# Kernel optimization log

Hardware: AMD Instinct MI355X
Metric: run time of the kernel (lower is better)

Reference implementation:

```python
import jax, jax.numpy as jnp
import numpy as np

NSIDE = 128
NLAT = 4 * NSIDE - 1          # 511 iso-latitude rings
NLON = 4 * NSIDE              # max pixels per ring (equatorial belt)
LMAX = NLAT                   # 511
MMAX = NLON // 2 + 1          # 257
NPIX = 12 * NSIDE * NSIDE     # 196608 HEALPix pixels (RING ordering)


def _healpix_geometry(nside, mmax):
    """Precompute per-ring synthesis tables for the irregular HEALPix iFFT.

    For ring k with nphi_k pixels and phase offset o_k, pixel longitudes are
    phi_{k,j} = 2*pi*(j + o_k)/nphi_k.  Real synthesis from one-sided spectrum:
        f_{k,j} = sum_m w_m * (Re(c_{k,m}) cos(m phi) - Im(c_{k,m}) sin(m phi)),
    w_0 = 1, w_m = 2 for m > 0 (irfft, norm='forward' convention as in
    torch-harmonics style SHT synthesis).  Returns dense [nlat, nlon, mmax]
    cos/sin tables masked to each ring's true length, plus the flat gather
    index mapping RING-ordered pixels into the padded [nlat, nlon] grid.
    """
    N = nside
    nlat, nlon = 4 * N - 1, 4 * N
    k = np.arange(nlat)
    # ring sizes: polar caps 4*i pixels, equatorial belt 4*N pixels
    nphi = np.where(k < N - 1, 4 * (k + 1),
                    np.where(k > 3 * N - 1, 4 * (4 * N - 1 - k), 4 * N))
    # phase offsets: caps shifted by half a pixel; belt alternates 1/2, 0
    off = np.where((k < N - 1) | (k > 3 * N - 1), 0.5,
                   np.where(((k - (N - 1)) % 2) == 0, 0.5, 0.0))
    j = np.arange(nlon)
    mask = (j[None, :] < nphi[:, None]).astype(np.float32)          # [nlat, nlon]
    phi = (2.0 * np.pi) * (j[None, :] + off[:, None]) / nphi[:, None]
    m = np.arange(mmax)
    w = np.where(m == 0, 1.0, 2.0).astype(np.float32)               # one-sided weights
    ang = (phi[:, :, None] * m[None, None, :]).astype(np.float32)   # [nlat, nlon, mmax]
    A = (w * np.cos(ang)) * mask[:, :, None]
    B = (-w * np.sin(ang)) * mask[:, :, None]
    # RING-ordered flat pixel -> (ring, j) -> padded-grid flat index
    starts = np.concatenate([[0], np.cumsum(nphi)[:-1]])
    ring = np.repeat(np.arange(nlat), nphi)
    jj = np.arange(int(nphi.sum())) - starts[ring]
    fidx = (ring * nlon + jj).astype(np.int32)
    return A.astype(np.float32), B.astype(np.float32), fidx


def setup_inputs() -> dict:
    key = jax.random.key(0)
    kx, kp = jax.random.split(key)
    # spectral coefficients, real view of complex [..., lmax, mmax]
    x = jax.random.normal(kx, (4, 16, LMAX, MMAX, 2), dtype=jnp.float32)
    # associated Legendre table buffer pct[m, l, k_ring] (random stand-in;
    # the real module precomputes normalized Legendre polynomials here)
    pct = jax.random.normal(kp, (MMAX, LMAX, NLAT), dtype=jnp.float32) * 0.05
    A, B, fidx = _healpix_geometry(NSIDE, MMAX)
    return {
        "x": x,
        "pct": pct,
        "A": jnp.asarray(A),
        "B": jnp.asarray(B),
        "fidx": jnp.asarray(fidx),
    }


def reference(x, pct, A, B, fidx):
    xr, xi = x[..., 0], x[..., 1]                       # [..., lmax, mmax]
    # Legendre contraction: '...lmn,mlk->...kmn' on the real view is simply
    # the same real contraction applied to Re and Im independently.
    Xr = jnp.einsum('...lm,mlk->...km', xr, pct)        # [..., nlat, mmax]
    Xi = jnp.einsum('...lm,mlk->...km', xi, pct)
    # irregular per-ring real iFFT synthesis on padded [nlat, nlon] grid
    grid = jnp.einsum('kjm,...km->...kj', A, Xr) + jnp.einsum('kjm,...km->...kj', B, Xi)
    flat = grid.reshape(grid.shape[:-2] + (NLAT * NLON,))
    return flat[..., fidx]                              # [..., npix] RING order
```

## Files before the change

### kernel.cpp

```cpp
#include <hip/hip_runtime.h>
#include <cstddef>

#define NSIDE_ 128
#define NLAT_  511
#define NLON_  512
#define LMAX_  511
#define MMAX_  257
#define NPIX_  196608
#define NB_    64
#define TWO_PI_ 6.28318530717958647692f

#define XELEMS_   16809856u
#define X2TELEMS_ 16842752u

typedef __attribute__((ext_vector_type(8))) short bf16x8;
typedef __attribute__((ext_vector_type(4))) float f32x4;

static __device__ __forceinline__ unsigned short f2bf(float f) {
    union { float f; unsigned int u; } v; v.f = f;
    unsigned int r = v.u + 0x7FFFu + ((v.u >> 16) & 1u);
    return (unsigned short)(r >> 16);
}

static __device__ __forceinline__ unsigned int cvtpk(float lo, float hi) {
    unsigned int d;
    asm("v_cvt_pk_bf16_f32 %0, %1, %2" : "=v"(d) : "v"(lo), "v"(hi));
    return d;
}

union U4V { uint4 u; bf16x8 v; };

static __device__ __forceinline__ bf16x8 ld_b64x2(const unsigned int* p) {
    union { struct { uint2 a, b; } s; bf16x8 v; } t;
    t.s.a = *(const uint2*)p;
    t.s.b = *(const uint2*)(p + 2);
    return t.v;
}

__global__ __launch_bounds__(256) void pack_x_k(
    const float* __restrict__ x, unsigned short* __restrict__ x2T)
{
    __shared__ unsigned short lds[32][520];
    int b   = blockIdx.x;
    int l0  = blockIdx.y * 32;
    int tid = threadIdx.x;

    const float* src = x + ((size_t)b * LMAX_ + l0) * (2 * MMAX_);
    for (int li = 0; li < 32; ++li) {
        bool valid = (l0 + li) < LMAX_;
        for (int m2 = tid; m2 < 2 * MMAX_; m2 += 256) {
            float f = valid ? src[(size_t)li * (2 * MMAX_) + m2] : 0.f;
            lds[li][m2] = f2bf(f);
        }
    }
    __syncthreads();

    for (int m2 = tid; m2 < 2 * MMAX_; m2 += 256) {
        int m  = m2 >> 1;
        int rb = (m2 & 1) * 64 + b;
        unsigned short* dst = x2T + ((size_t)m * 128 + rb) * 512 + l0;
#pragma unroll
        for (int g = 0; g < 4; ++g) {
            unsigned int w0 = (unsigned int)lds[g*8+0][m2] | ((unsigned int)lds[g*8+1][m2] << 16);
            unsigned int w1 = (unsigned int)lds[g*8+2][m2] | ((unsigned int)lds[g*8+3][m2] << 16);
            unsigned int w2 = (unsigned int)lds[g*8+4][m2] | ((unsigned int)lds[g*8+5][m2] << 16);
            unsigned int w3 = (unsigned int)lds[g*8+6][m2] | ((unsigned int)lds[g*8+7][m2] << 16);
            *(uint4*)(dst + g * 8) = make_uint4(w0, w1, w2, w3);
        }
    }
}

__global__ __launch_bounds__(256, 3) void legendre4_k(
    const unsigned short* __restrict__ x2T,
    const float* __restrict__ pct,
    float* __restrict__ X)
{
    int kt = blockIdx.x, m = blockIdx.y;
    int k0 = kt * 128;
    int lane = threadIdx.x & 63, w = threadIdx.x >> 6;
    int wk = (w >> 1) * 64, wrb = (w & 1) * 64;
    int r = lane & 15, g = lane >> 4;

    const float* pctm = pct + (size_t)m * (LMAX_ * NLAT_);
    const unsigned short* x2m = x2T + (size_t)m * (128 * 512);

    f32x4 acc[4][4];
#pragma unroll
    for (int a = 0; a < 4; ++a)
#pragma unroll
        for (int c = 0; c < 4; ++c) acc[a][c] = (f32x4){0.f, 0.f, 0.f, 0.f};

    int krow[4];
#pragma unroll
    for (int ks = 0; ks < 4; ++ks) {
        int k = k0 + wk + ks * 16 + r;
        krow[ks] = (k < NLAT_) ? k : (NLAT_ - 1);
    }

#pragma unroll 1
    for (int ls = 0; ls < 16; ++ls) {
        int lbase = ls * 32 + g * 8;

        bf16x8 Bf[4];
#pragma unroll
        for (int rs = 0; rs < 4; ++rs)
            Bf[rs] = *(const bf16x8*)(x2m + ((size_t)(wrb + rs * 16 + r) * 512 + lbase));

        bf16x8 Af[4];
#pragma unroll
        for (int ks = 0; ks < 4; ++ks) {
            float t[8];
#pragma unroll
            for (int i = 0; i < 8; ++i) {
                int l = lbase + i;
                if (l > LMAX_ - 1) l = LMAX_ - 1;
                t[i] = pctm[(size_t)l * NLAT_ + krow[ks]];
            }
            U4V uv;
            uv.u.x = cvtpk(t[0], t[1]);
            uv.u.y = cvtpk(t[2], t[3]);
            uv.u.z = cvtpk(t[4], t[5]);
            uv.u.w = cvtpk(t[6], t[7]);
            Af[ks] = uv.v;
        }

#pragma unroll
        for (int ks = 0; ks < 4; ++ks)
#pragma unroll
            for (int rs = 0; rs < 4; ++rs)
                acc[ks][rs] = __builtin_amdgcn_mfma_f32_16x16x32_bf16(
                    Af[ks], Bf[rs], acc[ks][rs], 0, 0, 0);
    }

    float wgt = (m == 0) ? 1.f : 2.f;
#pragma unroll
    for (int ks = 0; ks < 4; ++ks) {
#pragma unroll
        for (int rs = 0; rs < 4; ++rs) {
            int rb = wrb + rs * 16 + r;
#pragma unroll
            for (int i = 0; i < 4; ++i) {
                int k = k0 + wk + ks * 16 + g * 4 + i;
                if (k < NLAT_)
                    X[((size_t)k * MMAX_ + m) * 128 + rb] = acc[ks][rs][i] * wgt;
            }
        }
    }
}

__global__ __launch_bounds__(256, 3) void synth4_k(
    const float* __restrict__ X,
    float* __restrict__ out)
{
    __shared__ __align__(16) unsigned int Adw[256 * 18];
    __shared__ __align__(16) unsigned int Bdw[64 * 18];

    int k  = blockIdx.x;
    int jh = blockIdx.y;

    int nphi, start; float off;
    if (k < NSIDE_ - 1) {
        nphi  = 4 * (k + 1);
        start = 2 * k * (k + 1);
        off   = 0.5f;
    } else if (k <= 3 * NSIDE_ - 1) {
        nphi  = 4 * NSIDE_;
        start = 2 * (NSIDE_ - 1) * NSIDE_ + (k - (NSIDE_ - 1)) * 4 * NSIDE_;
        off   = (((k - (NSIDE_ - 1)) & 1) == 0) ? 0.5f : 0.f;
    } else {
        int t = NLAT_ - k;
        nphi  = 4 * t;
        start = NPIX_ - 2 * t * (t + 1);
        off   = 0.5f;
    }
    int jblk = jh * 256;
    if (jblk >= nphi) return;

    int tid  = threadIdx.x;
    int lane = tid & 63, w = tid >> 6;
    int r = lane & 15, g = lane >> 4;

    float theta = TWO_PI_ * ((float)(jblk + tid) + off) / (float)nphi;
    float dc, ds;
    sincosf(theta, &ds, &dc);
    float cs = 1.f, sn = 0.f;

    int bb = tid & 63, kq = tid >> 6;
    const float* Xk = X + (size_t)k * (MMAX_ * 128) + bb;
    float bv[8];
#pragma unroll
    for (int i = 0; i < 8; ++i) {
        int kap = kq * 8 + i;
        bv[i] = Xk[(size_t)(kap >> 1) * 128 + (kap & 1) * 64];
    }

    bool wact = (jblk + w * 64) < nphi;

    f32x4 acc[4][4];
#pragma unroll
    for (int a = 0; a < 4; ++a)
#pragma unroll
        for (int c = 0; c < 4; ++c) acc[a][c] = (f32x4){0.f, 0.f, 0.f, 0.f};

#pragma unroll 1
    for (int s = 0; s < 17; ++s) {
        unsigned int adw[16];
#pragma unroll
        for (int mi = 0; mi < 16; ++mi) {
            adw[mi] = cvtpk(cs, -sn);
            float cn = fmaf(cs, dc, -(sn * ds));
            float s2 = fmaf(sn, dc,  cs * ds);
            cs = cn; sn = s2;
        }
        unsigned int bdw[4];
#pragma unroll
        for (int q = 0; q < 4; ++q) bdw[q] = cvtpk(bv[2 * q], bv[2 * q + 1]);

        __syncthreads();
        {
            unsigned int* ap = Adw + tid * 18;
#pragma unroll
            for (int q = 0; q < 8; ++q)
                *(uint2*)(ap + 2 * q) = make_uint2(adw[2 * q], adw[2 * q + 1]);
            unsigned int* bp = Bdw + bb * 18 + kq * 4;
            *(uint2*)bp       = make_uint2(bdw[0], bdw[1]);
            *(uint2*)(bp + 2) = make_uint2(bdw[2], bdw[3]);
        }
        if (s + 1 < 17) {
            int kap0 = (s + 1) * 32 + kq * 8;
#pragma unroll
            for (int i = 0; i < 8; ++i) {
                int kap = kap0 + i;
                int mm  = kap >> 1;
                bv[i] = (mm < MMAX_) ? Xk[(size_t)mm * 128 + (kap & 1) * 64] : 0.f;
            }
        }
        __syncthreads();

        if (wact) {
            bf16x8 Af[4], Bf[4];
#pragma unroll
            for (int ks = 0; ks < 4; ++ks)
                Af[ks] = ld_b64x2(Adw + (w * 64 + ks * 16 + r) * 18 + g * 4);
#pragma unroll
            for (int bs = 0; bs < 4; ++bs)
                Bf[bs] = ld_b64x2(Bdw + (bs * 16 + r) * 18 + g * 4);
#pragma unroll
            for (int ks = 0; ks < 4; ++ks)
#pragma unroll
                for (int bs = 0; bs < 4; ++bs)
                    acc[ks][bs] = __builtin_amdgcn_mfma_f32_16x16x32_bf16(
                        Af[ks], Bf[bs], acc[ks][bs], 0, 0, 0);
        }
    }

    if (wact) {
#pragma unroll
        for (int ks = 0; ks < 4; ++ks)
#pragma unroll
            for (int bs = 0; bs < 4; ++bs) {
                int b = bs * 16 + r;
#pragma unroll
                for (int i = 0; i < 4; ++i) {
                    int j = jblk + w * 64 + ks * 16 + g * 4 + i;
                    if (j < nphi)
                        out[(size_t)b * NPIX_ + start + j] = acc[ks][bs][i];
                }
            }
    }
}

__global__ __launch_bounds__(256) void legendre_k(
    const float* __restrict__ x,
    const float* __restrict__ pct,
    float* __restrict__ X)
{
    int k  = blockIdx.x * 256 + threadIdx.x;
    int m  = blockIdx.y;
    int bh = blockIdx.z;
    bool active = (k < NLAT_);
    if (!active) k = NLAT_ - 1;

    float accR[32], accI[32];
#pragma unroll
    for (int i = 0; i < 32; ++i) { accR[i] = 0.f; accI[i] = 0.f; }

    const float* pcol  = pct + (size_t)m * LMAX_ * NLAT_ + k;
    const float* xbase = x + (size_t)(bh * 32) * LMAX_ * MMAX_ * 2 + (size_t)m * 2;
    const size_t bstride = (size_t)LMAX_ * MMAX_ * 2;

    for (int l = 0; l < LMAX_; ++l) {
        float p = pcol[(size_t)l * NLAT_];
        const float* xl = xbase + (size_t)l * MMAX_ * 2;
#pragma unroll
        for (int bb = 0; bb < 32; ++bb) {
            accR[bb] = fmaf(xl[(size_t)bb * bstride],     p, accR[bb]);
            accI[bb] = fmaf(xl[(size_t)bb * bstride + 1], p, accI[bb]);
        }
    }
    if (active) {
        float wv = (m == 0) ? 1.f : 2.f;
        size_t base = ((size_t)k * MMAX_ + m) * 128 + bh * 32;
#pragma unroll
        for (int bb = 0; bb < 32; ++bb) {
            X[base + bb]      = accR[bb] * wv;
            X[base + 64 + bb] = accI[bb] * wv;
        }
    }
}

__global__ __launch_bounds__(256) void synth2_k(
    const float* __restrict__ X,
    float* __restrict__ out)
{
    int k  = blockIdx.x;
    int j  = blockIdx.y * 256 + threadIdx.x;
    int bh = blockIdx.z;

    int nphi, start; float off;
    if (k < NSIDE_ - 1) {
        nphi  = 4 * (k + 1);
        start = 2 * k * (k + 1);
        off   = 0.5f;
    } else if (k <= 3 * NSIDE_ - 1) {
        nphi  = 4 * NSIDE_;
        start = 2 * (NSIDE_ - 1) * NSIDE_ + (k - (NSIDE_ - 1)) * 4 * NSIDE_;
        off   = (((k - (NSIDE_ - 1)) & 1) == 0) ? 0.5f : 0.f;
    } else {
        int t = NLAT_ - k;
        nphi  = 4 * t;
        start = NPIX_ - 2 * t * (t + 1);
        off   = 0.5f;
    }
    if (blockIdx.y == 1 && nphi <= 256) return;
    bool store_ok = (j < nphi);

    float ang = TWO_PI_ * ((float)j + off) / (float)nphi;
    float dsn, dcs;
    sincosf(ang, &dsn, &dcs);

    const float* Xk = X + (size_t)k * MMAX_ * 128 + bh * 32;

    float acc[32];
#pragma unroll
    for (int i = 0; i < 32; ++i) acc[i] = 0.f;

    float c = 1.f, s = 0.f;
    for (int m = 0; m < MMAX_; ++m) {
        const float* xm = Xk + (size_t)m * 128;
#pragma unroll
        for (int bb = 0; bb < 32; ++bb) {
            acc[bb] = fmaf(c, xm[bb], acc[bb]);
            acc[bb] = fmaf(-s, xm[64 + bb], acc[bb]);
        }
        float cn = fmaf(c, dcs, -(s * dsn));
        float s2 = fmaf(s, dcs,  (c * dsn));
        c = cn; s = s2;
    }

    if (store_ok) {
        float* op = out + (size_t)(bh * 32) * NPIX_ + start + j;
#pragma unroll
        for (int bb = 0; bb < 32; ++bb)
            op[(size_t)bb * NPIX_] = acc[bb];
    }
}

extern "C" void kernel_launch(void* const* d_in, const int* in_sizes, int n_in,
                              void* d_out, int out_size, void* d_ws, size_t ws_size,
                              hipStream_t stream)
{
    const float* x   = (const float*)d_in[0];
    const float* pct = (const float*)d_in[1];
    float* out = (float*)d_out;
    float* X   = (float*)d_ws;

    size_t need = (size_t)XELEMS_ * 4 + (size_t)X2TELEMS_ * 2;
    if (ws_size >= need) {
        unsigned short* x2T = (unsigned short*)(X + XELEMS_);
        pack_x_k<<<dim3(64, 16), dim3(256), 0, stream>>>(x, x2T);
        legendre4_k<<<dim3(4, MMAX_), dim3(256), 0, stream>>>(x2T, pct, X);
        synth4_k<<<dim3(NLAT_, 2), dim3(256), 0, stream>>>(X, out);
    } else {
        legendre_k<<<dim3(2, MMAX_, 2), dim3(256), 0, stream>>>(x, pct, X);
        synth2_k<<<dim3(NLAT_, 2, 2), dim3(256), 0, stream>>>(X, out);
    }
}
```

Before: 265.1 us.

## Stage Legendre table through swizzled LDS and double-buffer both GEMM kernels

The Legendre kernel now loads pct tiles with coalesced k-contiguous reads, packs them to bf16 in a double-buffered, XOR-swizzled LDS tile, and prefetches the next tile and x fragments while the MFMAs run. Blocks are remapped so consecutive m values spread across XCDs. The synthesis kernel double-buffers its A/B LDS tiles, drops one barrier per step, computes the next twiddle chunk while the current MFMAs run, and swizzles LDS columns to reduce bank conflicts. This removes strided uncoalesced pct gathers and barrier stalls, at the cost of more LDS and register pressure.

```diff
diff --git a/kernel.cpp b/kernel.cpp
--- a/kernel.cpp
+++ b/kernel.cpp
@@ -7,7 +7,6 @@
 #define LMAX_  511
 #define MMAX_  257
 #define NPIX_  196608
-#define NB_    64
 #define TWO_PI_ 6.28318530717958647692f
 
 #define XELEMS_   16809856u
@@ -28,9 +27,7 @@
     return d;
 }
 
-union U4V { uint4 u; bf16x8 v; };
-
-static __device__ __forceinline__ bf16x8 ld_b64x2(const unsigned int* p) {
+static __device__ __forceinline__ bf16x8 ld_pair(const unsigned int* p) {
     union { struct { uint2 a, b; } s; bf16x8 v; } t;
     t.s.a = *(const uint2*)p;
     t.s.b = *(const uint2*)(p + 2);
@@ -70,66 +67,97 @@
     }
 }
 
-__global__ __launch_bounds__(256, 3) void legendre4_k(
+__global__ __launch_bounds__(256, 3) void legendre5_k(
     const unsigned short* __restrict__ x2T,
     const float* __restrict__ pct,
     float* __restrict__ X)
 {
-    int kt = blockIdx.x, m = blockIdx.y;
-    int k0 = kt * 128;
-    int lane = threadIdx.x & 63, w = threadIdx.x >> 6;
+    __shared__ __align__(16) unsigned int Apk[2][128 * 18];
+
+    int bid = blockIdx.x;
+    int xcd = bid & 7, n = bid >> 3;
+    int kt = n & 3, mi = n >> 2;
+    int m = mi * 8 + xcd;
+    if (m >= MMAX_) return;
+
+    int k0  = kt * 128;
+    int tid = threadIdx.x;
+    int lane = tid & 63, w = tid >> 6;
     int wk = (w >> 1) * 64, wrb = (w & 1) * 64;
     int r = lane & 15, g = lane >> 4;
 
     const float* pctm = pct + (size_t)m * (LMAX_ * NLAT_);
     const unsigned short* x2m = x2T + (size_t)m * (128 * 512);
 
+    int kc = tid & 15;
+    int lp = tid >> 4;
+    int o7 = (k0 + kc + 112 <= NLAT_ - 1) ? 112 : (NLAT_ - 1 - (k0 + kc));
+
     f32x4 acc[4][4];
 #pragma unroll
     for (int a = 0; a < 4; ++a)
 #pragma unroll
         for (int c = 0; c < 4; ++c) acc[a][c] = (f32x4){0.f, 0.f, 0.f, 0.f};
 
-    int krow[4];
-#pragma unroll
-    for (int ks = 0; ks < 4; ++ks) {
-        int k = k0 + wk + ks * 16 + r;
-        krow[ks] = (k < NLAT_) ? k : (NLAT_ - 1);
-    }
-
-#pragma unroll 1
-    for (int ls = 0; ls < 16; ++ls) {
-        int lbase = ls * 32 + g * 8;
-
-        bf16x8 Bf[4];
+    float e0[8], e1[8];
+    bf16x8 Bfc[4], Bfn[4];
+
+    {
+        const float* pa = pctm + (size_t)(2 * lp)     * NLAT_ + k0 + kc;
+        const float* pb = pctm + (size_t)(2 * lp + 1) * NLAT_ + k0 + kc;
+#pragma unroll
+        for (int i = 0; i < 7; ++i) { e0[i] = pa[16 * i]; e1[i] = pb[16 * i]; }
+        e0[7] = pa[o7]; e1[7] = pb[o7];
 #pragma unroll
         for (int rs = 0; rs < 4; ++rs)
-            Bf[rs] = *(const bf16x8*)(x2m + ((size_t)(wrb + rs * 16 + r) * 512 + lbase));
-
+            Bfc[rs] = *(const bf16x8*)(x2m + (size_t)(wrb + rs * 16 + r) * 512 + g * 8);
+    }
+
+#pragma unroll 2
+    for (int s = 0; s < 16; ++s) {
+        const int bsel = s & 1;
+        unsigned int* wp = &Apk[bsel][0];
+#pragma unroll
+        for (int i = 0; i < 8; ++i) {
+            unsigned int dwv = cvtpk(e0[i], e1[i]);
+            int kk = kc + 16 * i;
+            wp[kk * 18 + (lp ^ ((i & 3) << 2))] = dwv;
+        }
+        __syncthreads();
+
+        if (s < 15) {
+            int l0n = (s + 1) * 32;
+            int la = l0n + 2 * lp, lb = la + 1;
+            if (lb > LMAX_ - 1) lb = LMAX_ - 1;
+            const float* pa = pctm + (size_t)la * NLAT_ + k0 + kc;
+            const float* pb = pctm + (size_t)lb * NLAT_ + k0 + kc;
+#pragma unroll
+            for (int i = 0; i < 7; ++i) { e0[i] = pa[16 * i]; e1[i] = pb[16 * i]; }
+            e0[7] = pa[o7]; e1[7] = pb[o7];
+            int lbase = l0n + g * 8;
+#pragma unroll
+            for (int rs = 0; rs < 4; ++rs)
+                Bfn[rs] = *(const bf16x8*)(x2m + (size_t)(wrb + rs * 16 + r) * 512 + lbase);
+        }
+
+        const unsigned int* rp = &Apk[bsel][0];
         bf16x8 Af[4];
 #pragma unroll
         for (int ks = 0; ks < 4; ++ks) {
-            float t[8];
-#pragma unroll
-            for (int i = 0; i < 8; ++i) {
-                int l = lbase + i;
-                if (l > LMAX_ - 1) l = LMAX_ - 1;
-                t[i] = pctm[(size_t)l * NLAT_ + krow[ks]];
-            }
-            U4V uv;
-            uv.u.x = cvtpk(t[0], t[1]);
-            uv.u.y = cvtpk(t[2], t[3]);
-            uv.u.z = cvtpk(t[4], t[5]);
-            uv.u.w = cvtpk(t[6], t[7]);
-            Af[ks] = uv.v;
-        }
-
+            int row = wk + ks * 16 + r;
+            Af[ks] = ld_pair(rp + row * 18 + ((g * 4) ^ ((ks & 3) << 2)));
+        }
 #pragma unroll
         for (int ks = 0; ks < 4; ++ks)
 #pragma unroll
             for (int rs = 0; rs < 4; ++rs)
                 acc[ks][rs] = __builtin_amdgcn_mfma_f32_16x16x32_bf16(
-                    Af[ks], Bf[rs], acc[ks][rs], 0, 0, 0);
+                    Af[ks], Bfc[rs], acc[ks][rs], 0, 0, 0);
+
+        if (s < 15) {
+#pragma unroll
+            for (int rs = 0; rs < 4; ++rs) Bfc[rs] = Bfn[rs];
+        }
     }
 
     float wgt = (m == 0) ? 1.f : 2.f;
@@ -148,12 +176,12 @@
     }
 }
 
-__global__ __launch_bounds__(256, 3) void synth4_k(
+__global__ __launch_bounds__(256, 3) void synth5_k(
     const float* __restrict__ X,
     float* __restrict__ out)
 {
-    __shared__ __align__(16) unsigned int Adw[256 * 18];
-    __shared__ __align__(16) unsigned int Bdw[64 * 18];
+    __shared__ __align__(16) unsigned int Adw[2][256 * 18];
+    __shared__ __align__(16) unsigned int Bdw[2][64 * 18];
 
     int k  = blockIdx.x;
     int jh = blockIdx.y;
@@ -187,12 +215,27 @@
 
     int bb = tid & 63, kq = tid >> 6;
     const float* Xk = X + (size_t)k * (MMAX_ * 128) + bb;
+
+    int swzA = ((tid >> 4) & 3) << 2;
+    int swzB = ((bb  >> 4) & 3) << 2;
+
     float bv[8];
 #pragma unroll
     for (int i = 0; i < 8; ++i) {
         int kap = kq * 8 + i;
         bv[i] = Xk[(size_t)(kap >> 1) * 128 + (kap & 1) * 64];
     }
+    unsigned int adw[16];
+#pragma unroll
+    for (int mi2 = 0; mi2 < 16; ++mi2) {
+        adw[mi2] = cvtpk(cs, -sn);
+        float cn = fmaf(cs, dc, -(sn * ds));
+        float s2 = fmaf(sn, dc,  cs * ds);
+        cs = cn; sn = s2;
+    }
+    unsigned int bdw[4];
+#pragma unroll
+    for (int q = 0; q < 4; ++q) bdw[q] = cvtpk(bv[2 * q], bv[2 * q + 1]);
 
     bool wact = (jblk + w * 64) < nphi;
 
@@ -202,31 +245,22 @@
 #pragma unroll
         for (int c = 0; c < 4; ++c) acc[a][c] = (f32x4){0.f, 0.f, 0.f, 0.f};
 
-#pragma unroll 1
+#pragma unroll 2
     for (int s = 0; s < 17; ++s) {
-        unsigned int adw[16];
-#pragma unroll
-        for (int mi = 0; mi < 16; ++mi) {
-            adw[mi] = cvtpk(cs, -sn);
-            float cn = fmaf(cs, dc, -(sn * ds));
-            float s2 = fmaf(sn, dc,  cs * ds);
-            cs = cn; sn = s2;
-        }
-        unsigned int bdw[4];
-#pragma unroll
-        for (int q = 0; q < 4; ++q) bdw[q] = cvtpk(bv[2 * q], bv[2 * q + 1]);
-
+        const int bsel = s & 1;
+        {
+            unsigned int* ap = &Adw[bsel][tid * 18];
+#pragma unroll
+            for (int q = 0; q < 8; ++q)
+                *(uint2*)(ap + ((2 * q) ^ swzA)) = make_uint2(adw[2 * q], adw[2 * q + 1]);
+            unsigned int* bp = &Bdw[bsel][bb * 18];
+            int cb = (kq * 4) ^ swzB;
+            *(uint2*)(bp + cb)     = make_uint2(bdw[0], bdw[1]);
+            *(uint2*)(bp + cb + 2) = make_uint2(bdw[2], bdw[3]);
+        }
         __syncthreads();
-        {
-            unsigned int* ap = Adw + tid * 18;
-#pragma unroll
-            for (int q = 0; q < 8; ++q)
-                *(uint2*)(ap + 2 * q) = make_uint2(adw[2 * q], adw[2 * q + 1]);
-            unsigned int* bp = Bdw + bb * 18 + kq * 4;
-            *(uint2*)bp       = make_uint2(bdw[0], bdw[1]);
-            *(uint2*)(bp + 2) = make_uint2(bdw[2], bdw[3]);
-        }
-        if (s + 1 < 17) {
+
+        if (s < 16) {
             int kap0 = (s + 1) * 32 + kq * 8;
 #pragma unroll
             for (int i = 0; i < 8; ++i) {
@@ -235,22 +269,41 @@
                 bv[i] = (mm < MMAX_) ? Xk[(size_t)mm * 128 + (kap & 1) * 64] : 0.f;
             }
         }
-        __syncthreads();
+        if (s < 16) {
+#pragma unroll
+            for (int mi2 = 0; mi2 < 16; ++mi2) {
+                adw[mi2] = cvtpk(cs, -sn);
+                float cn = fmaf(cs, dc, -(sn * ds));
+                float s2 = fmaf(sn, dc,  cs * ds);
+                cs = cn; sn = s2;
+            }
+        }
 
         if (wact) {
+            const unsigned int* arp = &Adw[bsel][0];
+            const unsigned int* brp = &Bdw[bsel][0];
             bf16x8 Af[4], Bf[4];
 #pragma unroll
-            for (int ks = 0; ks < 4; ++ks)
-                Af[ks] = ld_b64x2(Adw + (w * 64 + ks * 16 + r) * 18 + g * 4);
-#pragma unroll
-            for (int bs = 0; bs < 4; ++bs)
-                Bf[bs] = ld_b64x2(Bdw + (bs * 16 + r) * 18 + g * 4);
+            for (int ks = 0; ks < 4; ++ks) {
+                int row = w * 64 + ks * 16 + r;
+                Af[ks] = ld_pair(arp + row * 18 + ((g * 4) ^ ((ks & 3) << 2)));
+            }
+#pragma unroll
+            for (int bs = 0; bs < 4; ++bs) {
+                int row = bs * 16 + r;
+                Bf[bs] = ld_pair(brp + row * 18 + ((g * 4) ^ ((bs & 3) << 2)));
+            }
 #pragma unroll
             for (int ks = 0; ks < 4; ++ks)
 #pragma unroll
                 for (int bs = 0; bs < 4; ++bs)
                     acc[ks][bs] = __builtin_amdgcn_mfma_f32_16x16x32_bf16(
                         Af[ks], Bf[bs], acc[ks][bs], 0, 0, 0);
+        }
+
+        if (s < 16) {
+#pragma unroll
+            for (int q = 0; q < 4; ++q) bdw[q] = cvtpk(bv[2 * q], bv[2 * q + 1]);
         }
     }
 
@@ -379,8 +432,8 @@
     if (ws_size >= need) {
         unsigned short* x2T = (unsigned short*)(X + XELEMS_);
         pack_x_k<<<dim3(64, 16), dim3(256), 0, stream>>>(x, x2T);
-        legendre4_k<<<dim3(4, MMAX_), dim3(256), 0, stream>>>(x2T, pct, X);
-        synth4_k<<<dim3(NLAT_, 2), dim3(256), 0, stream>>>(X, out);
+        legendre5_k<<<dim3(1056), dim3(256), 0, stream>>>(x2T, pct, X);
+        synth5_k<<<dim3(NLAT_, 2), dim3(256), 0, stream>>>(X, out);
     } else {
         legendre_k<<<dim3(2, MMAX_, 2), dim3(256), 0, stream>>>(x, pct, X);
         synth2_k<<<dim3(NLAT_, 2, 2), dim3(256), 0, stream>>>(X, out);
```

Measured after the change: 214.1 us. -19.2%, faster.
